# Kernel tuning notes

Hardware: AMD Instinct MI355X
Metric: run time of the kernel (lower is better)

Reference implementation:

```python
import jax, jax.numpy as jnp
import numpy as np

SIZE_SUBMAP = 1024          # points per submap (module global in repo)
RATIO = 0.5                 # CONFIG['Detector']['ratio']
K_POS = int(SIZE_SUBMAP * RATIO)  # 512
K = 32                      # self.k, fps ratio = K / K_POS
B = 2048                    # number of submaps in batch


def fps_single(pts, k):
    """Deterministic farthest point sampling (start at index 0). pts: [n,3] -> [k] int indices."""
    min_d = jnp.sum((pts - pts[0]) ** 2, axis=-1)  # [n]

    def step(min_d, _):
        idx = jnp.argmax(min_d)
        d2 = jnp.sum((pts - pts[idx]) ** 2, axis=-1)
        return jnp.minimum(min_d, d2), idx

    _, idxs = jax.lax.scan(step, min_d, None, length=k - 1)
    return jnp.concatenate([jnp.zeros((1,), dtype=idxs.dtype), idxs])


def setup_inputs() -> dict:
    key = jax.random.key(0)
    ks = jax.random.split(key, 8)
    n = B * SIZE_SUBMAP
    x = jax.random.normal(ks[0], (n, 32), jnp.float32)
    pos = jax.random.normal(ks[1], (n, 3), jnp.float32) * 10.0
    batch = jnp.repeat(jnp.arange(B, dtype=jnp.int32), SIZE_SUBMAP)
    # MLP([32,16,8]) -> Linear(8,1) -> Softplus
    W1 = jax.random.normal(ks[2], (32, 16), jnp.float32) / np.sqrt(32.0)
    b1 = jnp.zeros((16,), jnp.float32)
    W2 = jax.random.normal(ks[3], (16, 8), jnp.float32) / np.sqrt(16.0)
    b2 = jnp.zeros((8,), jnp.float32)
    W3 = jax.random.normal(ks[4], (8, 1), jnp.float32) / np.sqrt(8.0)
    b3 = jnp.zeros((1,), jnp.float32)
    return {"x": x, "pos": pos, "batch": batch,
            "W1": W1, "b1": b1, "W2": W2, "b2": b2, "W3": W3, "b3": b3}


def reference(x, pos, batch, W1, b1, W2, b2, W3, b3):
    bsz = batch.shape[0] // SIZE_SUBMAP  # static batch_size (= batch.max()+1)
    # small per-point MLP + Softplus score
    h = jax.nn.relu(x @ W1 + b1)
    h = jax.nn.relu(h @ W2 + b2)
    s = jax.nn.softplus(h @ W3 + b3)          # [B*N, 1]
    x_batch = s.reshape(bsz, -1)               # [B, N]
    pos_b = pos.reshape(bsz, -1, 3)            # [B, N, 3]
    # distance of xy-coords to submap center
    dist = jnp.linalg.norm(pos_b[..., :2], axis=-1)     # [B, N]
    # k_pos closest points (topk of -dist)
    _, idx1 = jax.lax.top_k(-dist, K_POS)               # [B, K_POS]
    pos_sel = jnp.take_along_axis(pos_b, idx1[..., None], axis=1)  # [B, K_POS, 3]
    # batched farthest point sampling, K points per submap (within-batch indices)
    key_idx = jax.vmap(lambda p: fps_single(p, K))(pos_sel)        # [B, K]
    original_indices = jnp.take_along_axis(idx1, key_idx, axis=1)  # [B, K]
    weights = jnp.take_along_axis(x_batch, original_indices, axis=1)  # [B, K]
    return weights, original_indices
```

## Files before the change

kernel.cpp:

```cpp
#include <hip/hip_runtime.h>
#include <math.h>
#include <stdint.h>

#define N_PTS 1024
#define K_POS 512
#define K_FPS 32

typedef unsigned long long u64;
typedef unsigned int u32;

__device__ __forceinline__ u64 shfl_xor_u64(u64 v, int mask) {
    return __shfl_xor(v, mask, 64);
}

template<int J>
__device__ __forceinline__ void intra_stage(u64 key[16], int lane, int k) {
    #pragma unroll
    for (int r = 0; r < 16; ++r) {
        if ((r & J) == 0) {
            const int r2 = r | J;
            int p = (lane << 4) | r;
            bool up = ((p & k) == 0);
            u64 a = key[r], c = key[r2];
            bool sw = a < c;
            u64 lo = sw ? a : c;
            u64 hi = sw ? c : a;
            key[r]  = up ? lo : hi;
            key[r2] = up ? hi : lo;
        }
    }
}

__device__ __forceinline__ void cross_stage(u64 key[16], int lane, int m, int k) {
    bool low = ((lane & m) == 0);
    bool up  = ((lane & (k >> 4)) == 0);
    bool sel = (low == up);
    #pragma unroll
    for (int r = 0; r < 16; ++r) {
        u64 o = shfl_xor_u64(key[r], m);
        key[r] = ((key[r] < o) == sel) ? key[r] : o;
    }
}

__global__ __launch_bounds__(256) void sortfps_kernel(
    const float* __restrict__ pos,
    float* __restrict__ out_idx,
    int B)
{
#pragma clang fp contract(off)
    const int lane = threadIdx.x & 63;
    const int sub  = threadIdx.x >> 6;
    const int b    = blockIdx.x * 4 + sub;

    __shared__ float spts[4][N_PTS * 3];

    if (b >= B) return;

    const float* pb = pos + (size_t)b * N_PTS * 3;

    float4 f4[12];
    {
        const float4* pb4 = (const float4*)pb + (size_t)lane * 12;
        #pragma unroll
        for (int i = 0; i < 12; ++i) f4[i] = pb4[i];
        float4* sp4 = (float4*)&spts[sub][0] + lane * 12;
        #pragma unroll
        for (int i = 0; i < 12; ++i) sp4[i] = f4[i];
    }
    const float* f = (const float*)&f4[0];

    u64 key[16];
    #pragma unroll
    for (int r = 0; r < 16; ++r) {
        int p = (lane << 4) | r;
        float x = f[r * 3 + 0];
        float y = f[r * 3 + 1];
        float xx = x * x, yy = y * y;
        float d = sqrtf(xx + yy);
        key[r] = ((u64)__float_as_uint(d) << 32) | (u32)p;
    }

    intra_stage<1>(key, lane, 2);
    intra_stage<2>(key, lane, 4);
    intra_stage<1>(key, lane, 4);
    intra_stage<4>(key, lane, 8);
    intra_stage<2>(key, lane, 8);
    intra_stage<1>(key, lane, 8);
    intra_stage<8>(key, lane, 16);
    intra_stage<4>(key, lane, 16);
    intra_stage<2>(key, lane, 16);
    intra_stage<1>(key, lane, 16);
    #pragma unroll 1
    for (int k = 32; k <= N_PTS; k <<= 1) {
        #pragma unroll 1
        for (int j = k >> 1; j >= 16; j >>= 1)
            cross_stage(key, lane, j >> 4, k);
        intra_stage<8>(key, lane, k);
        intra_stage<4>(key, lane, k);
        intra_stage<2>(key, lane, k);
        intra_stage<1>(key, lane, k);
    }


    float px[16], py[16], pz[16], pidx[16], mind[16];
    #pragma unroll
    for (int r = 0; r < 16; ++r) {
        int orig = (int)(u32)(key[r] & 0xffffffffu);
        const float* sp = &spts[sub][orig * 3];
        px[r] = sp[0]; py[r] = sp[1]; pz[r] = sp[2];
        pidx[r] = (float)orig;
    }

    float* ob = out_idx + (size_t)b * K_FPS;
    float wx = __uint_as_float(__builtin_amdgcn_readlane(__float_as_uint(px[0]), 0));
    float wy = __uint_as_float(__builtin_amdgcn_readlane(__float_as_uint(py[0]), 0));
    float wz = __uint_as_float(__builtin_amdgcn_readlane(__float_as_uint(pz[0]), 0));
    if (lane == 0) ob[0] = pidx[0];

    #pragma unroll
    for (int r = 0; r < 16; ++r) {
        float dx = px[r] - wx, dy = py[r] - wy, dz = pz[r] - wz;
        float u0 = dx * dx, u1 = dy * dy, u2 = dz * dz;
        mind[r] = (u0 + u1) + u2;
    }
    if (lane >= 32) {
        #pragma unroll
        for (int r = 0; r < 16; ++r) mind[r] = -INFINITY;
    }

    for (int it = 1; it < K_FPS; ++it) {
        float bv = mind[0], bx = px[0], by = py[0], bz = pz[0], bi = pidx[0];
        #pragma unroll
        for (int r = 1; r < 16; ++r) {
            bool g = mind[r] > bv;
            bv = g ? mind[r] : bv;
            bx = g ? px[r] : bx;
            by = g ? py[r] : by;
            bz = g ? pz[r] : bz;
            bi = g ? pidx[r] : bi;
        }
        int bvi = __float_as_int(bv);
        int g = bvi;
        #pragma unroll
        for (int m = 1; m <= 16; m <<= 1) {
            int o = __shfl_xor(g, m, 64);
            g = (o > g) ? o : g;
        }
        u64 mask = __ballot(bvi == g) & 0xffffffffull;
        int W = __ffsll((unsigned long long)mask) - 1;
        wx = __uint_as_float(__builtin_amdgcn_readlane(__float_as_uint(bx), W));
        wy = __uint_as_float(__builtin_amdgcn_readlane(__float_as_uint(by), W));
        wz = __uint_as_float(__builtin_amdgcn_readlane(__float_as_uint(bz), W));
        float wi = __uint_as_float(__builtin_amdgcn_readlane(__float_as_uint(bi), W));
        if (lane == 0) ob[it] = wi;

        #pragma unroll
        for (int r = 0; r < 16; ++r) {
            float dx = px[r] - wx, dy = py[r] - wy, dz = pz[r] - wz;
            float u0 = dx * dx, u1 = dy * dy, u2 = dz * dz;
            float d2 = (u0 + u1) + u2;
            mind[r] = fminf(mind[r], d2);
        }
    }
}

__global__ __launch_bounds__(256) void mlp_kernel(
    const float* __restrict__ x,
    const float* __restrict__ W1, const float* __restrict__ b1,
    const float* __restrict__ W2, const float* __restrict__ b2,
    const float* __restrict__ W3, const float* __restrict__ b3,
    const float* __restrict__ idx_f,
    float* __restrict__ out_w, int total)
{
    __shared__ float sW1[32 * 16];
    __shared__ float sW2[16 * 8];
    __shared__ float sW3[8];
    __shared__ float sb1[16];
    __shared__ float sb2[8];
    __shared__ float sb3;

    for (int i = threadIdx.x; i < 512; i += 256) sW1[i] = W1[i];
    if (threadIdx.x < 128) sW2[threadIdx.x] = W2[threadIdx.x];
    if (threadIdx.x < 16)  sb1[threadIdx.x] = b1[threadIdx.x];
    if (threadIdx.x < 8) {
        sb2[threadIdx.x] = b2[threadIdx.x];
        sW3[threadIdx.x] = W3[threadIdx.x];
    }
    if (threadIdx.x == 0) sb3 = b3[0];
    __syncthreads();

    int t = blockIdx.x * 256 + threadIdx.x;
    if (t >= total) return;

    int b    = t >> 5;
    int orig = (int)(idx_f[t] + 0.5f);
    const float* xr = x + ((size_t)b * N_PTS + (size_t)orig) * 32;

    float xi[32];
    #pragma unroll
    for (int i = 0; i < 32; i += 4) {
        float4 v = *(const float4*)(xr + i);
        xi[i] = v.x; xi[i + 1] = v.y; xi[i + 2] = v.z; xi[i + 3] = v.w;
    }

    float h1[16];
    #pragma unroll
    for (int j = 0; j < 16; ++j) {
        float a = sb1[j];
        #pragma unroll
        for (int i = 0; i < 32; ++i) a += xi[i] * sW1[i * 16 + j];
        h1[j] = fmaxf(a, 0.0f);
    }
    float h2[8];
    #pragma unroll
    for (int j = 0; j < 8; ++j) {
        float a = sb2[j];
        #pragma unroll
        for (int i = 0; i < 16; ++i) a += h1[i] * sW2[i * 8 + j];
        h2[j] = fmaxf(a, 0.0f);
    }
    float v = sb3;
    #pragma unroll
    for (int i = 0; i < 8; ++i) v += h2[i] * sW3[i];

    float sp = fmaxf(v, 0.0f) + log1pf(expf(-fabsf(v)));
    out_w[t] = sp;
}

extern "C" void kernel_launch(void* const* d_in, const int* in_sizes, int n_in,
                              void* d_out, int out_size, void* d_ws, size_t ws_size,
                              hipStream_t stream) {
    const float* x   = (const float*)d_in[0];
    const float* pos = (const float*)d_in[1];
    const float* W1 = (const float*)d_in[3];
    const float* b1 = (const float*)d_in[4];
    const float* W2 = (const float*)d_in[5];
    const float* b2 = (const float*)d_in[6];
    const float* W3 = (const float*)d_in[7];
    const float* b3 = (const float*)d_in[8];

    const int B = in_sizes[2] / N_PTS;
    float* out_w = (float*)d_out;
    float* out_i = (float*)d_out + (size_t)B * K_FPS;

    sortfps_kernel<<<(B + 3) / 4, 256, 0, stream>>>(pos, out_i, B);

    const int total = B * K_FPS;
    mlp_kernel<<<(total + 255) / 256, 256, 0, stream>>>(
        x, W1, b1, W2, b2, W3, b3, out_i, out_w, total);
}
```

Baseline: 382.1 us.

## Split per-submap bitonic sort across two waves with DPP shuffles and LDS merge

Each submap now gets a 128-thread block (two wavefronts) holding 8 keys per lane instead of one wave with 16, so each thread carries half the sort registers. Small-distance cross-lane exchanges use DPP and ds_swizzle instead of generic shuffles, and the two sorted halves are merged through LDS before the second wave exits. The FPS loop uses a tree argmax over 8 elements, a DPP row reduction for the wave max, and reads the winner's coordinates from LDS. It also writes all indices in a single store at the end. The risk is the extra __syncthreads and an idle second wave during FPS, traded against higher occupancy and shorter dependency chains.

```diff
diff --git a/kernel.cpp b/kernel.cpp
--- a/kernel.cpp
+++ b/kernel.cpp
@@ -3,7 +3,6 @@
 #include <stdint.h>
 
 #define N_PTS 1024
-#define K_POS 512
 #define K_FPS 32
 
 typedef unsigned long long u64;
@@ -13,66 +12,97 @@
     return __shfl_xor(v, mask, 64);
 }
 
+__device__ __forceinline__ int imax2(int a, int b) { return a > b ? a : b; }
+
+template<int CTRL, int RM>
+__device__ __forceinline__ int dpp_upd(int v) {
+    return __builtin_amdgcn_update_dpp(0, v, CTRL, RM, 0xf, true);
+}
+
+template<int M>
+__device__ __forceinline__ u64 xshfl(u64 v) {
+    if constexpr (M == 32) {
+        return shfl_xor_u64(v, 32);
+    } else {
+        u32 lo = (u32)v, hi = (u32)(v >> 32);
+        if constexpr (M == 1) {
+            lo = (u32)dpp_upd<0xB1, 0xf>((int)lo);
+            hi = (u32)dpp_upd<0xB1, 0xf>((int)hi);
+        } else if constexpr (M == 2) {
+            lo = (u32)dpp_upd<0x4E, 0xf>((int)lo);
+            hi = (u32)dpp_upd<0x4E, 0xf>((int)hi);
+        } else {
+            constexpr int imm = (M << 10) | 0x1F;
+            lo = (u32)__builtin_amdgcn_ds_swizzle((int)lo, imm);
+            hi = (u32)__builtin_amdgcn_ds_swizzle((int)hi, imm);
+        }
+        return ((u64)hi << 32) | lo;
+    }
+}
+
 template<int J>
-__device__ __forceinline__ void intra_stage(u64 key[16], int lane, int k) {
-    #pragma unroll
-    for (int r = 0; r < 16; ++r) {
+__device__ __forceinline__ void intra8(u64 key[8], int L, int k) {
+    #pragma unroll
+    for (int r = 0; r < 8; ++r) {
         if ((r & J) == 0) {
             const int r2 = r | J;
-            int p = (lane << 4) | r;
+            int p = (L << 3) | r;
             bool up = ((p & k) == 0);
             u64 a = key[r], c = key[r2];
             bool sw = a < c;
-            u64 lo = sw ? a : c;
-            u64 hi = sw ? c : a;
-            key[r]  = up ? lo : hi;
-            key[r2] = up ? hi : lo;
+            u64 lo2 = sw ? a : c;
+            u64 hi2 = sw ? c : a;
+            key[r]  = up ? lo2 : hi2;
+            key[r2] = up ? hi2 : lo2;
         }
     }
 }
 
-__device__ __forceinline__ void cross_stage(u64 key[16], int lane, int m, int k) {
-    bool low = ((lane & m) == 0);
-    bool up  = ((lane & (k >> 4)) == 0);
+template<int M>
+__device__ __forceinline__ void cross8(u64 key[8], int L, int k) {
+    bool low = ((L & M) == 0);
+    bool up  = ((L & (k >> 3)) == 0);
     bool sel = (low == up);
     #pragma unroll
-    for (int r = 0; r < 16; ++r) {
-        u64 o = shfl_xor_u64(key[r], m);
+    for (int r = 0; r < 8; ++r) {
+        u64 o = xshfl<M>(key[r]);
         key[r] = ((key[r] < o) == sel) ? key[r] : o;
     }
 }
 
-__global__ __launch_bounds__(256) void sortfps_kernel(
+__global__ __launch_bounds__(128) void sortfps_kernel(
     const float* __restrict__ pos,
     float* __restrict__ out_idx,
     int B)
 {
 #pragma clang fp contract(off)
-    const int lane = threadIdx.x & 63;
-    const int sub  = threadIdx.x >> 6;
-    const int b    = blockIdx.x * 4 + sub;
-
-    __shared__ float spts[4][N_PTS * 3];
+    const int t    = threadIdx.x;
+    const int lane = t & 63;
+    const int wv   = t >> 6;
+    const int b    = blockIdx.x;
+
+    __shared__ __attribute__((aligned(16))) float spts[N_PTS * 3];
+    __shared__ u64 xch[512];
 
     if (b >= B) return;
 
     const float* pb = pos + (size_t)b * N_PTS * 3;
 
-    float4 f4[12];
+    float4 f4[6];
     {
-        const float4* pb4 = (const float4*)pb + (size_t)lane * 12;
-        #pragma unroll
-        for (int i = 0; i < 12; ++i) f4[i] = pb4[i];
-        float4* sp4 = (float4*)&spts[sub][0] + lane * 12;
-        #pragma unroll
-        for (int i = 0; i < 12; ++i) sp4[i] = f4[i];
+        const float4* pb4 = (const float4*)pb + (size_t)t * 6;
+        #pragma unroll
+        for (int i = 0; i < 6; ++i) f4[i] = pb4[i];
+        float4* sp4 = (float4*)spts + t * 6;
+        #pragma unroll
+        for (int i = 0; i < 6; ++i) sp4[i] = f4[i];
     }
     const float* f = (const float*)&f4[0];
 
-    u64 key[16];
-    #pragma unroll
-    for (int r = 0; r < 16; ++r) {
-        int p = (lane << 4) | r;
+    u64 key[8];
+    #pragma unroll
+    for (int r = 0; r < 8; ++r) {
+        int p = (t << 3) | r;
         float x = f[r * 3 + 0];
         float y = f[r * 3 + 1];
         float xx = x * x, yy = y * y;
@@ -80,88 +110,110 @@
         key[r] = ((u64)__float_as_uint(d) << 32) | (u32)p;
     }
 
-    intra_stage<1>(key, lane, 2);
-    intra_stage<2>(key, lane, 4);
-    intra_stage<1>(key, lane, 4);
-    intra_stage<4>(key, lane, 8);
-    intra_stage<2>(key, lane, 8);
-    intra_stage<1>(key, lane, 8);
-    intra_stage<8>(key, lane, 16);
-    intra_stage<4>(key, lane, 16);
-    intra_stage<2>(key, lane, 16);
-    intra_stage<1>(key, lane, 16);
-    #pragma unroll 1
-    for (int k = 32; k <= N_PTS; k <<= 1) {
-        #pragma unroll 1
-        for (int j = k >> 1; j >= 16; j >>= 1)
-            cross_stage(key, lane, j >> 4, k);
-        intra_stage<8>(key, lane, k);
-        intra_stage<4>(key, lane, k);
-        intra_stage<2>(key, lane, k);
-        intra_stage<1>(key, lane, k);
-    }
-
-
-    float px[16], py[16], pz[16], pidx[16], mind[16];
-    #pragma unroll
-    for (int r = 0; r < 16; ++r) {
-        int orig = (int)(u32)(key[r] & 0xffffffffu);
-        const float* sp = &spts[sub][orig * 3];
+    intra8<1>(key, t, 2);
+    intra8<2>(key, t, 4);  intra8<1>(key, t, 4);
+    intra8<4>(key, t, 8);  intra8<2>(key, t, 8);  intra8<1>(key, t, 8);
+
+    cross8<1>(key, t, 16);
+    intra8<4>(key, t, 16); intra8<2>(key, t, 16); intra8<1>(key, t, 16);
+
+    cross8<2>(key, t, 32); cross8<1>(key, t, 32);
+    intra8<4>(key, t, 32); intra8<2>(key, t, 32); intra8<1>(key, t, 32);
+
+    cross8<4>(key, t, 64); cross8<2>(key, t, 64); cross8<1>(key, t, 64);
+    intra8<4>(key, t, 64); intra8<2>(key, t, 64); intra8<1>(key, t, 64);
+
+    cross8<8>(key, t, 128); cross8<4>(key, t, 128); cross8<2>(key, t, 128);
+    cross8<1>(key, t, 128);
+    intra8<4>(key, t, 128); intra8<2>(key, t, 128); intra8<1>(key, t, 128);
+
+    cross8<16>(key, t, 256); cross8<8>(key, t, 256); cross8<4>(key, t, 256);
+    cross8<2>(key, t, 256);  cross8<1>(key, t, 256);
+    intra8<4>(key, t, 256); intra8<2>(key, t, 256); intra8<1>(key, t, 256);
+
+    cross8<32>(key, t, 512); cross8<16>(key, t, 512); cross8<8>(key, t, 512);
+    cross8<4>(key, t, 512);  cross8<2>(key, t, 512);  cross8<1>(key, t, 512);
+    intra8<4>(key, t, 512); intra8<2>(key, t, 512); intra8<1>(key, t, 512);
+
+    if (wv == 1) {
+        #pragma unroll
+        for (int r = 0; r < 8; ++r) xch[r * 64 + lane] = key[r];
+    }
+    __syncthreads();
+    if (wv == 1) return;
+
+    #pragma unroll
+    for (int r = 0; r < 8; ++r) {
+        u64 o = xch[r * 64 + lane];
+        key[r] = key[r] < o ? key[r] : o;
+    }
+    cross8<32>(key, t, 1024); cross8<16>(key, t, 1024); cross8<8>(key, t, 1024);
+    cross8<4>(key, t, 1024);  cross8<2>(key, t, 1024);  cross8<1>(key, t, 1024);
+    intra8<4>(key, t, 1024); intra8<2>(key, t, 1024); intra8<1>(key, t, 1024);
+
+
+    float px[8], py[8], pz[8], pidx[8], mind[8];
+    #pragma unroll
+    for (int r = 0; r < 8; ++r) {
+        int o = (int)(u32)key[r];
+        const float* sp = &spts[o * 3];
         px[r] = sp[0]; py[r] = sp[1]; pz[r] = sp[2];
-        pidx[r] = (float)orig;
+        pidx[r] = (float)o;
     }
 
     float* ob = out_idx + (size_t)b * K_FPS;
-    float wx = __uint_as_float(__builtin_amdgcn_readlane(__float_as_uint(px[0]), 0));
-    float wy = __uint_as_float(__builtin_amdgcn_readlane(__float_as_uint(py[0]), 0));
-    float wz = __uint_as_float(__builtin_amdgcn_readlane(__float_as_uint(pz[0]), 0));
-    if (lane == 0) ob[0] = pidx[0];
-
-    #pragma unroll
-    for (int r = 0; r < 16; ++r) {
+    int o0 = __builtin_amdgcn_readfirstlane((int)(u32)key[0]);
+    float wx = spts[o0 * 3], wy = spts[o0 * 3 + 1], wz = spts[o0 * 3 + 2];
+    float acc = (float)o0;
+
+    #pragma unroll
+    for (int r = 0; r < 8; ++r) {
         float dx = px[r] - wx, dy = py[r] - wy, dz = pz[r] - wz;
         float u0 = dx * dx, u1 = dy * dy, u2 = dz * dz;
         mind[r] = (u0 + u1) + u2;
     }
-    if (lane >= 32) {
-        #pragma unroll
-        for (int r = 0; r < 16; ++r) mind[r] = -INFINITY;
-    }
 
     for (int it = 1; it < K_FPS; ++it) {
-        float bv = mind[0], bx = px[0], by = py[0], bz = pz[0], bi = pidx[0];
-        #pragma unroll
-        for (int r = 1; r < 16; ++r) {
-            bool g = mind[r] > bv;
-            bv = g ? mind[r] : bv;
-            bx = g ? px[r] : bx;
-            by = g ? py[r] : by;
-            bz = g ? pz[r] : bz;
-            bi = g ? pidx[r] : bi;
+        float v4[4], i4[4];
+        #pragma unroll
+        for (int q = 0; q < 4; ++q) {
+            bool g = mind[2 * q + 1] > mind[2 * q];
+            v4[q] = g ? mind[2 * q + 1] : mind[2 * q];
+            i4[q] = g ? pidx[2 * q + 1] : pidx[2 * q];
         }
+        bool s01 = v4[1] > v4[0];
+        float va = s01 ? v4[1] : v4[0], ia = s01 ? i4[1] : i4[0];
+        bool s23 = v4[3] > v4[2];
+        float vb = s23 ? v4[3] : v4[2], ib = s23 ? i4[3] : i4[2];
+        bool sab = vb > va;
+        float bv = sab ? vb : va, bi = sab ? ib : ia;
+
         int bvi = __float_as_int(bv);
         int g = bvi;
-        #pragma unroll
-        for (int m = 1; m <= 16; m <<= 1) {
-            int o = __shfl_xor(g, m, 64);
-            g = (o > g) ? o : g;
-        }
-        u64 mask = __ballot(bvi == g) & 0xffffffffull;
+        g = imax2(g, dpp_upd<0x111, 0xf>(g));
+        g = imax2(g, dpp_upd<0x112, 0xf>(g));
+        g = imax2(g, dpp_upd<0x114, 0xf>(g));
+        g = imax2(g, dpp_upd<0x118, 0xf>(g));
+        g = imax2(g, dpp_upd<0x142, 0xa>(g));
+        g = imax2(g, dpp_upd<0x143, 0xc>(g));
+        int gmax = __builtin_amdgcn_readlane(g, 63);
+
+        u64 mask = __ballot(bvi == gmax);
         int W = __ffsll((unsigned long long)mask) - 1;
-        wx = __uint_as_float(__builtin_amdgcn_readlane(__float_as_uint(bx), W));
-        wy = __uint_as_float(__builtin_amdgcn_readlane(__float_as_uint(by), W));
-        wz = __uint_as_float(__builtin_amdgcn_readlane(__float_as_uint(bz), W));
         float wi = __uint_as_float(__builtin_amdgcn_readlane(__float_as_uint(bi), W));
-        if (lane == 0) ob[it] = wi;
-
-        #pragma unroll
-        for (int r = 0; r < 16; ++r) {
+        int wo = (int)wi;
+        wx = spts[wo * 3]; wy = spts[wo * 3 + 1]; wz = spts[wo * 3 + 2];
+        if (lane == it) acc = wi;
+
+        #pragma unroll
+        for (int r = 0; r < 8; ++r) {
             float dx = px[r] - wx, dy = py[r] - wy, dz = pz[r] - wz;
             float u0 = dx * dx, u1 = dy * dy, u2 = dz * dz;
             float d2 = (u0 + u1) + u2;
             mind[r] = fminf(mind[r], d2);
         }
     }
+    if (lane < K_FPS) ob[lane] = acc;
 }
 
 __global__ __launch_bounds__(256) void mlp_kernel(
@@ -243,7 +295,7 @@
     float* out_w = (float*)d_out;
     float* out_i = (float*)d_out + (size_t)B * K_FPS;
 
-    sortfps_kernel<<<(B + 3) / 4, 256, 0, stream>>>(pos, out_i, B);
+    sortfps_kernel<<<B, 128, 0, stream>>>(pos, out_i, B);
 
     const int total = B * K_FPS;
     mlp_kernel<<<(total + 255) / 256, 256, 0, stream>>>(
```

Result: faster. 365.2 us (-4.4%).
